# Kernel optimization log

Measured on AMD Instinct MI355X. Metric: run time of the kernel, lower is better.

The kernel has to match this reference:

```python
import jax, jax.numpy as jnp
import numpy as np

B = 2097152   # batch
L = 5         # latent_size
H = 16        # mlp_size
P = 2         # param_size
CLS = 3       # closure input size: concat([Y, x1, x2])


def _init_linear(key, fan_in, fan_out):
    kw, kb = jax.random.split(key)
    bound = 1.0 / np.sqrt(fan_in)
    W = jax.random.uniform(kw, (fan_in, fan_out), jnp.float32, -bound, bound)
    b = jax.random.uniform(kb, (fan_out,), jnp.float32, -bound, bound)
    return W, b


def setup_inputs() -> dict:
    key = jax.random.key(0)
    ks = jax.random.split(key, 10)
    inputs = jax.random.normal(ks[0], (B, 2), jnp.float32)
    Z = jax.random.normal(ks[1], (B, L), jnp.float32)
    Y = jax.random.normal(ks[2], (B, 1), jnp.float32)
    # nn.Parameter(torch.zeros(L, L)) in the original; use small random so the
    # matmul path is numerically non-trivial for kernel testing.
    A = jax.random.normal(ks[3], (L, L), jnp.float32) * 0.1
    w2a, b2a = _init_linear(ks[4], L, H)
    w2b, b2b = _init_linear(ks[5], H, H)
    w2c, b2c = _init_linear(ks[6], H, P)
    wfa, bfa = _init_linear(ks[7], CLS, H)
    wfb, bfb = _init_linear(ks[8], H, H)
    wfc, bfc = _init_linear(ks[9], H, 1)
    return dict(inputs=inputs, Z=Z, Y=Y, A=A,
                w2a=w2a, b2a=b2a, w2b=w2b, b2b=b2b, w2c=w2c, b2c=b2c,
                wfa=wfa, bfa=bfa, wfb=wfb, bfb=bfb, wfc=wfc, bfc=bfc)


def reference(inputs, Z, Y, A, w2a, b2a, w2b, b2b, w2c, b2c,
              wfa, bfa, wfb, bfb, wfc, bfc):
    x1 = inputs[:, 0:1]
    x2 = inputs[:, 1:2]
    c = 0.0  # self.switch defaults to 0

    new_Z = Z @ A                                   # [B, L]
    # mlp2: L -> H -> H -> P with ReLU on hidden layers
    h = jax.nn.relu(new_Z @ w2a + b2a)
    h = jax.nn.relu(h @ w2b + b2b)
    K = jnp.abs(h @ w2c + b2c)                      # [B, P]
    k1 = K[:, 0:1]
    k2 = K[:, 1:2]

    # closure MLP f[0]: concat([Y, x1, x2]) -> 1 (multiplied by switch c)
    fin = jnp.concatenate([Y, x1, x2], axis=-1)     # [B, 3]
    g = jax.nn.relu(fin @ wfa + bfa)
    g = jax.nn.relu(g @ wfb + bfb)
    g = g @ wfc + bfc                               # [B, 1]

    DY = -Y + k1 * x1 - k2 * x2 + c * g
    new_S = Y + DY
    # original returns (Y + DY, [new_Z, new_S])
    return (new_S, new_Z, new_S)
```

## Files before the change

### kernel.cpp

```cpp
#include <hip/hip_runtime.h>


#define LDIM 5
#define HDIM 16

constexpr int BLOCK = 256;
constexpr int R = 4;

__global__ __launch_bounds__(BLOCK) void lpsc_kernel(
    const float* __restrict__ inputs,
    const float* __restrict__ Zin,
    const float* __restrict__ Yin,
    const float* __restrict__ A,
    const float* __restrict__ w2a,
    const float* __restrict__ b2a,
    const float* __restrict__ w2b,
    const float* __restrict__ b2b,
    const float* __restrict__ w2c,
    const float* __restrict__ b2c,
    float* __restrict__ out,
    int B)
{
    const int t = threadIdx.x;
    const long long g = (long long)blockIdx.x * BLOCK + t;
    const long long r0 = g * R;
    if (r0 >= B) return;
    const bool full = (r0 + R <= B);

    float z[R][LDIM];
    float x1[R], x2[R], y[R];

    if (full) {
        const float4 iv0 = reinterpret_cast<const float4*>(inputs)[g * 2 + 0];
        const float4 iv1 = reinterpret_cast<const float4*>(inputs)[g * 2 + 1];
        x1[0] = iv0.x; x2[0] = iv0.y; x1[1] = iv0.z; x2[1] = iv0.w;
        x1[2] = iv1.x; x2[2] = iv1.y; x1[3] = iv1.z; x2[3] = iv1.w;
        const float4 yv = reinterpret_cast<const float4*>(Yin)[g];
        y[0] = yv.x; y[1] = yv.y; y[2] = yv.z; y[3] = yv.w;
        float zf[R * LDIM];
        #pragma unroll
        for (int q = 0; q < 5; ++q) {
            const float4 zv = reinterpret_cast<const float4*>(Zin)[g * 5 + q];
            zf[q * 4 + 0] = zv.x; zf[q * 4 + 1] = zv.y;
            zf[q * 4 + 2] = zv.z; zf[q * 4 + 3] = zv.w;
        }
        #pragma unroll
        for (int r = 0; r < R; ++r)
            #pragma unroll
            for (int k = 0; k < LDIM; ++k) z[r][k] = zf[r * LDIM + k];
    } else {
        #pragma unroll
        for (int r = 0; r < R; ++r) {
            long long rr = (r0 + r < B) ? (r0 + r) : (long long)(B - 1);
            x1[r] = inputs[rr * 2 + 0];
            x2[r] = inputs[rr * 2 + 1];
            y[r]  = Yin[rr];
            #pragma unroll
            for (int k = 0; k < LDIM; ++k) z[r][k] = Zin[rr * LDIM + k];
        }
    }

    float nz[R][LDIM];
    #pragma unroll
    for (int r = 0; r < R; ++r)
        #pragma unroll
        for (int j = 0; j < LDIM; ++j) nz[r][j] = 0.0f;
    #pragma unroll
    for (int k = 0; k < LDIM; ++k)
        #pragma unroll
        for (int j = 0; j < LDIM; ++j) {
            const float a = A[k * LDIM + j];
            #pragma unroll
            for (int r = 0; r < R; ++r) nz[r][j] = fmaf(z[r][k], a, nz[r][j]);
        }

    float h[R][HDIM];
    #pragma unroll
    for (int r = 0; r < R; ++r)
        #pragma unroll
        for (int j = 0; j < HDIM; ++j) h[r][j] = b2a[j];
    #pragma unroll
    for (int k = 0; k < LDIM; ++k)
        #pragma unroll
        for (int j = 0; j < HDIM; ++j) {
            const float w = w2a[k * HDIM + j];
            #pragma unroll
            for (int r = 0; r < R; ++r) h[r][j] = fmaf(nz[r][k], w, h[r][j]);
        }
    #pragma unroll
    for (int r = 0; r < R; ++r)
        #pragma unroll
        for (int j = 0; j < HDIM; ++j) h[r][j] = fmaxf(h[r][j], 0.0f);

    float g2[R][HDIM];
    #pragma unroll
    for (int r = 0; r < R; ++r)
        #pragma unroll
        for (int j = 0; j < HDIM; ++j) g2[r][j] = b2b[j];
    #pragma unroll
    for (int k = 0; k < HDIM; ++k)
        #pragma unroll
        for (int j = 0; j < HDIM; ++j) {
            const float w = w2b[k * HDIM + j];
            #pragma unroll
            for (int r = 0; r < R; ++r) g2[r][j] = fmaf(h[r][k], w, g2[r][j]);
        }
    #pragma unroll
    for (int r = 0; r < R; ++r)
        #pragma unroll
        for (int j = 0; j < HDIM; ++j) g2[r][j] = fmaxf(g2[r][j], 0.0f);

    float k1[R], k2[R];
    #pragma unroll
    for (int r = 0; r < R; ++r) { k1[r] = b2c[0]; k2[r] = b2c[1]; }
    #pragma unroll
    for (int k = 0; k < HDIM; ++k) {
        const float w0 = w2c[k * 2 + 0];
        const float w1 = w2c[k * 2 + 1];
        #pragma unroll
        for (int r = 0; r < R; ++r) {
            k1[r] = fmaf(g2[r][k], w0, k1[r]);
            k2[r] = fmaf(g2[r][k], w1, k2[r]);
        }
    }

    float ns[R];
    #pragma unroll
    for (int r = 0; r < R; ++r) {
        const float K1 = fabsf(k1[r]);
        const float K2 = fabsf(k2[r]);
        const float dy = -y[r] + K1 * x1[r] - K2 * x2[r];
        ns[r] = y[r] + dy;
    }

    if (full) {
        float4 nsv = make_float4(ns[0], ns[1], ns[2], ns[3]);
        reinterpret_cast<float4*>(out)[g] = nsv;
        reinterpret_cast<float4*>(out + (long long)6 * B)[g] = nsv;
        float zf[R * LDIM];
        #pragma unroll
        for (int r = 0; r < R; ++r)
            #pragma unroll
            for (int j = 0; j < LDIM; ++j) zf[r * LDIM + j] = nz[r][j];
        #pragma unroll
        for (int q = 0; q < 5; ++q) {
            reinterpret_cast<float4*>(out + (long long)B)[g * 5 + q] =
                make_float4(zf[q * 4 + 0], zf[q * 4 + 1], zf[q * 4 + 2], zf[q * 4 + 3]);
        }
    } else {
        #pragma unroll
        for (int r = 0; r < R; ++r) {
            const long long row = r0 + r;
            if (row < B) {
                out[row] = ns[r];
                out[(long long)6 * B + row] = ns[r];
                #pragma unroll
                for (int j = 0; j < LDIM; ++j)
                    out[(long long)B + row * LDIM + j] = nz[r][j];
            }
        }
    }
}

extern "C" void kernel_launch(void* const* d_in, const int* in_sizes, int n_in,
                              void* d_out, int out_size, void* d_ws, size_t ws_size,
                              hipStream_t stream) {
    const float* inputs = (const float*)d_in[0];
    const float* Zin    = (const float*)d_in[1];
    const float* Yin    = (const float*)d_in[2];
    const float* A      = (const float*)d_in[3];
    const float* w2a    = (const float*)d_in[4];
    const float* b2a    = (const float*)d_in[5];
    const float* w2b    = (const float*)d_in[6];
    const float* b2b    = (const float*)d_in[7];
    const float* w2c    = (const float*)d_in[8];
    const float* b2c    = (const float*)d_in[9];

    const int B = in_sizes[2];
    const int rowsPerBlock = BLOCK * R;
    const int grid = (B + rowsPerBlock - 1) / rowsPerBlock;

    lpsc_kernel<<<grid, BLOCK, 0, stream>>>(inputs, Zin, Yin, A, w2a, b2a,
                                            w2b, b2b, w2c, b2c,
                                            (float*)d_out, B);
}
```

Baseline: 158.3 us.

## Process two rows per thread with 8-byte vector accesses and nontemporal stores

Each thread now handles two rows instead of four, loading and storing through 2-wide float vectors, and the stores are marked nontemporal. An odd leftover row goes to a separate small tail kernel. The aim is more threads and waves in flight to hide memory latency, plus less register pressure per thread and less cache pollution from the streaming writes. In exchange the accesses are narrower, so more memory instructions are issued per byte moved.

```diff
diff --git a/kernel.cpp b/kernel.cpp
--- a/kernel.cpp
+++ b/kernel.cpp
@@ -3,163 +3,130 @@
 
 #define LDIM 5
 #define HDIM 16
+constexpr int BLOCK = 256;
 
-constexpr int BLOCK = 256;
-constexpr int R = 4;
+typedef float f32x2 __attribute__((ext_vector_type(2)));
+typedef float f32x4 __attribute__((ext_vector_type(4)));
 
-__global__ __launch_bounds__(BLOCK) void lpsc_kernel(
+__device__ __forceinline__ void lpsc_row(
+    const float* __restrict__ z,
+    const float* __restrict__ A,
+    const float* __restrict__ w2a, const float* __restrict__ b2a,
+    const float* __restrict__ w2b, const float* __restrict__ b2b,
+    const float* __restrict__ w2c, const float* __restrict__ b2c,
+    float x1, float x2, float y,
+    float* __restrict__ nz_out, float* __restrict__ ns_out)
+{
+    float nz[LDIM];
+    #pragma unroll
+    for (int j = 0; j < LDIM; ++j) nz[j] = 0.0f;
+    #pragma unroll
+    for (int k = 0; k < LDIM; ++k)
+        #pragma unroll
+        for (int j = 0; j < LDIM; ++j)
+            nz[j] = fmaf(z[k], A[k * LDIM + j], nz[j]);
+
+    float h[HDIM];
+    #pragma unroll
+    for (int j = 0; j < HDIM; ++j) h[j] = b2a[j];
+    #pragma unroll
+    for (int k = 0; k < LDIM; ++k)
+        #pragma unroll
+        for (int j = 0; j < HDIM; ++j)
+            h[j] = fmaf(nz[k], w2a[k * HDIM + j], h[j]);
+    #pragma unroll
+    for (int j = 0; j < HDIM; ++j) h[j] = fmaxf(h[j], 0.0f);
+
+    float g2[HDIM];
+    #pragma unroll
+    for (int j = 0; j < HDIM; ++j) g2[j] = b2b[j];
+    #pragma unroll
+    for (int k = 0; k < HDIM; ++k)
+        #pragma unroll
+        for (int j = 0; j < HDIM; ++j)
+            g2[j] = fmaf(h[k], w2b[k * HDIM + j], g2[j]);
+    #pragma unroll
+    for (int j = 0; j < HDIM; ++j) g2[j] = fmaxf(g2[j], 0.0f);
+
+    float k1 = b2c[0], k2 = b2c[1];
+    #pragma unroll
+    for (int k = 0; k < HDIM; ++k) {
+        k1 = fmaf(g2[k], w2c[k * 2 + 0], k1);
+        k2 = fmaf(g2[k], w2c[k * 2 + 1], k2);
+    }
+    const float K1 = fabsf(k1);
+    const float K2 = fabsf(k2);
+    *ns_out = y + (-y + K1 * x1 - K2 * x2);
+    #pragma unroll
+    for (int j = 0; j < LDIM; ++j) nz_out[j] = nz[j];
+}
+
+__global__ __launch_bounds__(BLOCK) void lpsc_main(
     const float* __restrict__ inputs,
     const float* __restrict__ Zin,
     const float* __restrict__ Yin,
     const float* __restrict__ A,
-    const float* __restrict__ w2a,
-    const float* __restrict__ b2a,
-    const float* __restrict__ w2b,
-    const float* __restrict__ b2b,
-    const float* __restrict__ w2c,
-    const float* __restrict__ b2c,
+    const float* __restrict__ w2a, const float* __restrict__ b2a,
+    const float* __restrict__ w2b, const float* __restrict__ b2b,
+    const float* __restrict__ w2c, const float* __restrict__ b2c,
     float* __restrict__ out,
-    int B)
+    unsigned B, unsigned pairs)
 {
-    const int t = threadIdx.x;
-    const long long g = (long long)blockIdx.x * BLOCK + t;
-    const long long r0 = g * R;
-    if (r0 >= B) return;
-    const bool full = (r0 + R <= B);
+    const unsigned g = blockIdx.x * (unsigned)BLOCK + threadIdx.x;
+    if (g >= pairs) return;
 
-    float z[R][LDIM];
-    float x1[R], x2[R], y[R];
-
-    if (full) {
-        const float4 iv0 = reinterpret_cast<const float4*>(inputs)[g * 2 + 0];
-        const float4 iv1 = reinterpret_cast<const float4*>(inputs)[g * 2 + 1];
-        x1[0] = iv0.x; x2[0] = iv0.y; x1[1] = iv0.z; x2[1] = iv0.w;
-        x1[2] = iv1.x; x2[2] = iv1.y; x1[3] = iv1.z; x2[3] = iv1.w;
-        const float4 yv = reinterpret_cast<const float4*>(Yin)[g];
-        y[0] = yv.x; y[1] = yv.y; y[2] = yv.z; y[3] = yv.w;
-        float zf[R * LDIM];
-        #pragma unroll
-        for (int q = 0; q < 5; ++q) {
-            const float4 zv = reinterpret_cast<const float4*>(Zin)[g * 5 + q];
-            zf[q * 4 + 0] = zv.x; zf[q * 4 + 1] = zv.y;
-            zf[q * 4 + 2] = zv.z; zf[q * 4 + 3] = zv.w;
-        }
-        #pragma unroll
-        for (int r = 0; r < R; ++r)
-            #pragma unroll
-            for (int k = 0; k < LDIM; ++k) z[r][k] = zf[r * LDIM + k];
-    } else {
-        #pragma unroll
-        for (int r = 0; r < R; ++r) {
-            long long rr = (r0 + r < B) ? (r0 + r) : (long long)(B - 1);
-            x1[r] = inputs[rr * 2 + 0];
-            x2[r] = inputs[rr * 2 + 1];
-            y[r]  = Yin[rr];
-            #pragma unroll
-            for (int k = 0; k < LDIM; ++k) z[r][k] = Zin[rr * LDIM + k];
-        }
+    const f32x4 iv = reinterpret_cast<const f32x4*>(inputs)[g];
+    const f32x2 yv = reinterpret_cast<const f32x2*>(Yin)[g];
+    float zl[2 * LDIM];
+    const f32x2* zp = reinterpret_cast<const f32x2*>(Zin) + (size_t)g * LDIM;
+    #pragma unroll
+    for (int q = 0; q < LDIM; ++q) {
+        const f32x2 v = zp[q];
+        zl[2 * q] = v.x;
+        zl[2 * q + 1] = v.y;
     }
 
-    float nz[R][LDIM];
+    float nz0[LDIM], nz1[LDIM], ns0, ns1;
+    lpsc_row(&zl[0],    A, w2a, b2a, w2b, b2b, w2c, b2c, iv.x, iv.y, yv.x, nz0, &ns0);
+    lpsc_row(&zl[LDIM], A, w2a, b2a, w2b, b2b, w2c, b2c, iv.z, iv.w, yv.y, nz1, &ns1);
+
+    const f32x2 nsv = {ns0, ns1};
+    __builtin_nontemporal_store(nsv, reinterpret_cast<f32x2*>(out) + g);
+    __builtin_nontemporal_store(nsv, reinterpret_cast<f32x2*>(out + (size_t)6 * B) + g);
+    f32x2* oz = reinterpret_cast<f32x2*>(out + (size_t)B) + (size_t)g * LDIM;
+    const f32x2 z0 = {nz0[0], nz0[1]};
+    const f32x2 z1 = {nz0[2], nz0[3]};
+    const f32x2 z2 = {nz0[4], nz1[0]};
+    const f32x2 z3 = {nz1[1], nz1[2]};
+    const f32x2 z4 = {nz1[3], nz1[4]};
+    __builtin_nontemporal_store(z0, oz + 0);
+    __builtin_nontemporal_store(z1, oz + 1);
+    __builtin_nontemporal_store(z2, oz + 2);
+    __builtin_nontemporal_store(z3, oz + 3);
+    __builtin_nontemporal_store(z4, oz + 4);
+}
+
+__global__ void lpsc_tail(
+    const float* __restrict__ inputs, const float* __restrict__ Zin,
+    const float* __restrict__ Yin, const float* __restrict__ A,
+    const float* __restrict__ w2a, const float* __restrict__ b2a,
+    const float* __restrict__ w2b, const float* __restrict__ b2b,
+    const float* __restrict__ w2c, const float* __restrict__ b2c,
+    float* __restrict__ out, unsigned B, unsigned start)
+{
+    const unsigned row = start + blockIdx.x * blockDim.x + threadIdx.x;
+    if (row >= B) return;
+    float z[LDIM];
     #pragma unroll
-    for (int r = 0; r < R; ++r)
-        #pragma unroll
-        for (int j = 0; j < LDIM; ++j) nz[r][j] = 0.0f;
+    for (int k = 0; k < LDIM; ++k) z[k] = Zin[(size_t)row * LDIM + k];
+    float nz[LDIM], ns;
+    lpsc_row(z, A, w2a, b2a, w2b, b2b, w2c, b2c,
+             inputs[(size_t)row * 2 + 0], inputs[(size_t)row * 2 + 1], Yin[row],
+             nz, &ns);
+    out[row] = ns;
+    out[(size_t)6 * B + row] = ns;
     #pragma unroll
-    for (int k = 0; k < LDIM; ++k)
-        #pragma unroll
-        for (int j = 0; j < LDIM; ++j) {
-            const float a = A[k * LDIM + j];
-            #pragma unroll
-            for (int r = 0; r < R; ++r) nz[r][j] = fmaf(z[r][k], a, nz[r][j]);
-        }
-
-    float h[R][HDIM];
-    #pragma unroll
-    for (int r = 0; r < R; ++r)
-        #pragma unroll
-        for (int j = 0; j < HDIM; ++j) h[r][j] = b2a[j];
-    #pragma unroll
-    for (int k = 0; k < LDIM; ++k)
-        #pragma unroll
-        for (int j = 0; j < HDIM; ++j) {
-            const float w = w2a[k * HDIM + j];
-            #pragma unroll
-            for (int r = 0; r < R; ++r) h[r][j] = fmaf(nz[r][k], w, h[r][j]);
-        }
-    #pragma unroll
-    for (int r = 0; r < R; ++r)
-        #pragma unroll
-        for (int j = 0; j < HDIM; ++j) h[r][j] = fmaxf(h[r][j], 0.0f);
-
-    float g2[R][HDIM];
-    #pragma unroll
-    for (int r = 0; r < R; ++r)
-        #pragma unroll
-        for (int j = 0; j < HDIM; ++j) g2[r][j] = b2b[j];
-    #pragma unroll
-    for (int k = 0; k < HDIM; ++k)
-        #pragma unroll
-        for (int j = 0; j < HDIM; ++j) {
-            const float w = w2b[k * HDIM + j];
-            #pragma unroll
-            for (int r = 0; r < R; ++r) g2[r][j] = fmaf(h[r][k], w, g2[r][j]);
-        }
-    #pragma unroll
-    for (int r = 0; r < R; ++r)
-        #pragma unroll
-        for (int j = 0; j < HDIM; ++j) g2[r][j] = fmaxf(g2[r][j], 0.0f);
-
-    float k1[R], k2[R];
-    #pragma unroll
-    for (int r = 0; r < R; ++r) { k1[r] = b2c[0]; k2[r] = b2c[1]; }
-    #pragma unroll
-    for (int k = 0; k < HDIM; ++k) {
-        const float w0 = w2c[k * 2 + 0];
-        const float w1 = w2c[k * 2 + 1];
-        #pragma unroll
-        for (int r = 0; r < R; ++r) {
-            k1[r] = fmaf(g2[r][k], w0, k1[r]);
-            k2[r] = fmaf(g2[r][k], w1, k2[r]);
-        }
-    }
-
-    float ns[R];
-    #pragma unroll
-    for (int r = 0; r < R; ++r) {
-        const float K1 = fabsf(k1[r]);
-        const float K2 = fabsf(k2[r]);
-        const float dy = -y[r] + K1 * x1[r] - K2 * x2[r];
-        ns[r] = y[r] + dy;
-    }
-
-    if (full) {
-        float4 nsv = make_float4(ns[0], ns[1], ns[2], ns[3]);
-        reinterpret_cast<float4*>(out)[g] = nsv;
-        reinterpret_cast<float4*>(out + (long long)6 * B)[g] = nsv;
-        float zf[R * LDIM];
-        #pragma unroll
-        for (int r = 0; r < R; ++r)
-            #pragma unroll
-            for (int j = 0; j < LDIM; ++j) zf[r * LDIM + j] = nz[r][j];
-        #pragma unroll
-        for (int q = 0; q < 5; ++q) {
-            reinterpret_cast<float4*>(out + (long long)B)[g * 5 + q] =
-                make_float4(zf[q * 4 + 0], zf[q * 4 + 1], zf[q * 4 + 2], zf[q * 4 + 3]);
-        }
-    } else {
-        #pragma unroll
-        for (int r = 0; r < R; ++r) {
-            const long long row = r0 + r;
-            if (row < B) {
-                out[row] = ns[r];
-                out[(long long)6 * B + row] = ns[r];
-                #pragma unroll
-                for (int j = 0; j < LDIM; ++j)
-                    out[(long long)B + row * LDIM + j] = nz[r][j];
-            }
-        }
-    }
+    for (int j = 0; j < LDIM; ++j) out[(size_t)B + (size_t)row * LDIM + j] = nz[j];
 }
 
 extern "C" void kernel_launch(void* const* d_in, const int* in_sizes, int n_in,
@@ -176,11 +143,16 @@
     const float* w2c    = (const float*)d_in[8];
     const float* b2c    = (const float*)d_in[9];
 
-    const int B = in_sizes[2];
-    const int rowsPerBlock = BLOCK * R;
-    const int grid = (B + rowsPerBlock - 1) / rowsPerBlock;
+    const unsigned B = (unsigned)in_sizes[2];
+    const unsigned pairs = B / 2;
+    const unsigned grid = (pairs + BLOCK - 1) / BLOCK;
 
-    lpsc_kernel<<<grid, BLOCK, 0, stream>>>(inputs, Zin, Yin, A, w2a, b2a,
-                                            w2b, b2b, w2c, b2c,
-                                            (float*)d_out, B);
+    lpsc_main<<<grid, BLOCK, 0, stream>>>(inputs, Zin, Yin, A, w2a, b2a,
+                                          w2b, b2b, w2c, b2c,
+                                          (float*)d_out, B, pairs);
+    if (B & 1u) {
+        lpsc_tail<<<1, 64, 0, stream>>>(inputs, Zin, Yin, A, w2a, b2a,
+                                        w2b, b2b, w2c, b2c,
+                                        (float*)d_out, B, pairs * 2);
+    }
 }
```

After: 145.4 us. 8.2% less time.
